# Kernel tuning notes

Measured on AMD Instinct MI355X. Metric: run time of the kernel, lower is better.

## Reference

```python
import jax, jax.numpy as jnp
import numpy as np

B = 4          # per_gpu_batch_size
P = 16         # n_contexts
N = B * P      # fused passage dim = 64
L = 512        # seq_len
H = 768        # hidden_size
S = 16         # sentence spans per passage


def setup_inputs() -> dict:
    key = jax.random.key(0)
    k1, k2, k3 = jax.random.split(key, 3)
    hidden_states = jax.random.normal(k1, (N, L, H), jnp.float32)
    # nn.Linear weight [out, in]; original init std=1.0 saturates tanh, use 0.02 scale for sane numerics
    dense_w = jax.random.normal(k2, (H, H), jnp.float32) * 0.02
    dense_b = jnp.zeros((H,), jnp.float32)
    attention_mask = jnp.ones((N, L), jnp.int32)
    # strictly increasing boundaries -> S non-empty, ragged, contiguous spans per passage
    r = jnp.sort(jax.random.randint(k3, (N, S + 1), 0, L - S), axis=-1) + jnp.arange(S + 1, dtype=jnp.int32)
    spans = jnp.stack([r[:, :-1], r[:, 1:]], axis=-1).astype(jnp.int32)  # [N, S, 2]
    return dict(hidden_states=hidden_states, dense_w=dense_w, dense_b=dense_b,
                attention_mask=attention_mask, spans=spans)


def reference(hidden_states, dense_w, dense_b, attention_mask, spans):
    # sentence_spans branch: token_tensor = hidden_states (all tokens)
    # pooled_output = activation(dense(token_tensor)); cls_norm_type == 'none' -> no norm
    pooled = jnp.tanh(jnp.einsum('nlh,oh->nlo', hidden_states, dense_w) + dense_b)  # [N, L, H]
    pooled_output_passages = pooled[:, 0]  # [N, H]
    # ragged per-span mean pooling, vectorized as a masked segment reduce
    pos = jnp.arange(L, dtype=jnp.int32)                         # [L]
    start = spans[..., 0][..., None]                             # [N, S, 1]
    end = spans[..., 1][..., None]                               # [N, S, 1]
    m = ((pos >= start) & (pos < end)).astype(pooled.dtype)      # [N, S, L]
    sums = jnp.einsum('nsl,nlh->nsh', m, pooled)                 # [N, S, H]
    counts = (spans[..., 1] - spans[..., 0]).astype(pooled.dtype)[..., None]  # [N, S, 1]
    sentence_embeddings = (sums / counts).reshape(N * S, H)      # [N*S, H]
    # all S spans valid per passage -> mask of zeros (0 = valid in original code)
    sentence_mask = jnp.zeros((N, S), jnp.float32)
    return pooled_output_passages, sentence_embeddings, sentence_mask
```

## Files before the change

### kernel.cpp

```cpp
#include <hip/hip_runtime.h>
#include <hip/hip_bf16.h>

#define NPASS 64
#define LSEQ  512
#define HDIM  768
#define NSPAN 16
#define MTOT  (NPASS*LSEQ)
#define OFF_SENT (NPASS*HDIM)
#define OFF_MASK (OFF_SENT + NPASS*NSPAN*HDIM)
#define A_ELEMS (MTOT*HDIM)

#define BN   96
#define NTN  6
#define BK   32
#define NK   (HDIM/BK)
#define NTILES (HDIM/BN)
#define NBLK (NPASS*NTILES)
#define THREADS 512
#define NMT  4

typedef __bf16 bf16x8 __attribute__((ext_vector_type(8)));
typedef __bf16 bf16x4 __attribute__((ext_vector_type(4)));
typedef float  f32x4  __attribute__((ext_vector_type(4)));

__device__ inline unsigned short f2bf(float f) {
  __hip_bfloat16 h = __float2bfloat16(f);
  unsigned short u; __builtin_memcpy(&u, &h, 2); return u;
}

__device__ inline float fast_tanh(float x) {
  const float ax = fabsf(x);
  const float t  = __expf(-2.0f * ax);
  const float r  = (1.0f - t) * __builtin_amdgcn_rcpf(1.0f + t);
  return copysignf(r, x);
}

__device__ inline bf16x8 cvt8(f32x4 lo, f32x4 hi) {
  union { bf16x4 h[2]; bf16x8 v; } u;
  u.h[0] = __builtin_convertvector(lo, bf16x4);
  u.h[1] = __builtin_convertvector(hi, bf16x4);
  return u.v;
}

__global__ __launch_bounds__(256) void convert_a_kernel(
    const float* __restrict__ A, unsigned short* __restrict__ Ab)
{
  const long long i = ((long long)blockIdx.x * 256 + threadIdx.x) * 8;
  const float4 a = *(const float4*)(A + i);
  const float4 b = *(const float4*)(A + i + 4);
  union { unsigned short us[8]; uint4 v; } o;
  o.us[0]=f2bf(a.x); o.us[1]=f2bf(a.y); o.us[2]=f2bf(a.z); o.us[3]=f2bf(a.w);
  o.us[4]=f2bf(b.x); o.us[5]=f2bf(b.y); o.us[6]=f2bf(b.z); o.us[7]=f2bf(b.w);
  *(uint4*)(Ab + i) = o.v;
}

__global__ __launch_bounds__(THREADS, 2) void fused_kernel(
    const unsigned short* __restrict__ Ab,
    const float* __restrict__ W,
    const float* __restrict__ bias,
    const int*   __restrict__ spans,
    float* __restrict__ out)
{
  __shared__ __align__(16) unsigned short Wl[BN * HDIM];
  __shared__ float sent_lds[NSPAN][BN];
  __shared__ float inv_s[NSPAN];
  __shared__ float bias_s[BN];
  __shared__ short sid_l[LSEQ];

  const int tid = threadIdx.x;
  const int b   = blockIdx.x;
  const int xcd = b & 7;
  const int t   = b >> 3;
  const int p   = ((t >> 3) << 3) | xcd;
  const int ntb = t & 7;
  const int tile_n = ntb * BN;


  {
    const float* Wp = W + (size_t)tile_n * HDIM;
    #pragma unroll
    for (int j = 0; j < (BN * (HDIM / 8)) / THREADS; ++j) {
      const int g  = j * THREADS + tid;
      const int wr = g / (HDIM / 8);
      const int kg = g % (HDIM / 8);
      const float* src = Wp + (size_t)wr * HDIM + kg * 8;
      const f32x4 lo = *(const f32x4*)src;
      const f32x4 hi = *(const f32x4*)(src + 4);
      const int kgs = kg ^ (wr & 7);
      *(bf16x8*)(Wl + (size_t)wr * HDIM + kgs * 8) = cvt8(lo, hi);
    }
  }

  {
    int st[NSPAN], en[NSPAN];
    #pragma unroll
    for (int i = 0; i < NSPAN; ++i) {
      st[i] = spans[(p * NSPAN + i) * 2 + 0];
      en[i] = spans[(p * NSPAN + i) * 2 + 1];
    }
    short s = -1;
    #pragma unroll
    for (int i = 0; i < NSPAN; ++i)
      if (tid >= st[i] && tid < en[i]) s = (short)i;
    sid_l[tid] = s;
  }
  if (tid < NSPAN)
    inv_s[tid] = 1.0f / (float)(spans[(p * NSPAN + tid) * 2 + 1] -
                                spans[(p * NSPAN + tid) * 2 + 0]);
  if (tid < BN) bias_s[tid] = bias[tile_n + tid];
  for (int i = tid; i < NSPAN * BN; i += THREADS) (&sent_lds[0][0])[i] = 0.f;

  __syncthreads();

  const int wave = tid >> 6;
  const int lane = tid & 63;
  const int quad = lane >> 4;
  const int lr   = lane & 15;

  const unsigned short* Abp =
      Ab + ((size_t)p * LSEQ + wave * 64 + lr) * HDIM + quad * 8;

  f32x4 acc[NMT][NTN];
  #pragma unroll
  for (int mt = 0; mt < NMT; ++mt)
    #pragma unroll
    for (int nt = 0; nt < NTN; ++nt)
      acc[mt][nt] = (f32x4){0.f, 0.f, 0.f, 0.f};

  bf16x8 a_cur[NMT], a_nxt[NMT];
  #pragma unroll
  for (int mt = 0; mt < NMT; ++mt)
    a_cur[mt] = *(const bf16x8*)(Abp + (size_t)mt * 16 * HDIM);

  #pragma unroll
  for (int k = 0; k < NK; ++k) {
    bf16x8 wf[NTN];
    #pragma unroll
    for (int nt = 0; nt < NTN; ++nt) {
      const int wr = nt * 16 + lr;
      const int kg = (4 * k + quad) ^ (lr & 7);
      wf[nt] = *(const bf16x8*)(Wl + (size_t)wr * HDIM + kg * 8);
    }
    if (k + 1 < NK) {
      #pragma unroll
      for (int mt = 0; mt < NMT; ++mt)
        a_nxt[mt] = *(const bf16x8*)(Abp + (size_t)mt * 16 * HDIM + (k + 1) * BK);
    }
    __builtin_amdgcn_s_setprio(1);
    #pragma unroll
    for (int mt = 0; mt < NMT; ++mt)
      #pragma unroll
      for (int nt = 0; nt < NTN; ++nt)
        acc[mt][nt] = __builtin_amdgcn_mfma_f32_16x16x32_bf16(
            a_cur[mt], wf[nt], acc[mt][nt], 0, 0, 0);
    __builtin_amdgcn_s_setprio(0);
    #pragma unroll
    for (int mt = 0; mt < NMT; ++mt) a_cur[mt] = a_nxt[mt];
  }

  #pragma unroll
  for (int nt = 0; nt < NTN; ++nt) {
    const int col = nt * 16 + lr;
    const float bv = bias_s[col];
    #pragma unroll
    for (int mt = 0; mt < NMT; ++mt) {
      const int rowbase = wave * 64 + mt * 16 + quad * 4;
      int prev = -1; float run = 0.f;
      #pragma unroll
      for (int r = 0; r < 4; ++r) {
        const int row = rowbase + r;
        const float v = fast_tanh(acc[mt][nt][r] + bv);
        if (row == 0) out[(size_t)p * HDIM + tile_n + col] = v;
        const int s = sid_l[row];
        if (s != prev) {
          if (prev >= 0) atomicAdd(&sent_lds[prev][col], run);
          prev = s; run = 0.f;
        }
        run += v;
      }
      if (prev >= 0) atomicAdd(&sent_lds[prev][col], run);
    }
  }
  __syncthreads();

  for (int i = tid; i < NSPAN * BN; i += THREADS) {
    const int s = i / BN, c = i % BN;
    out[OFF_SENT + ((size_t)p * NSPAN + s) * HDIM + tile_n + c] =
        sent_lds[s][c] * inv_s[s];
  }
  if (ntb == 0 && tid < NSPAN) out[OFF_MASK + p * NSPAN + tid] = 0.f;
}

extern "C" void kernel_launch(void* const* d_in, const int* in_sizes, int n_in,
                              void* d_out, int out_size, void* d_ws, size_t ws_size,
                              hipStream_t stream) {
  const float* hs  = (const float*)d_in[0];
  const float* w   = (const float*)d_in[1];
  const float* bsc = (const float*)d_in[2];
  const int* spans = (const int*)d_in[4];

  unsigned short* Ab = (unsigned short*)d_ws;

  convert_a_kernel<<<dim3(A_ELEMS / 8 / 256), dim3(256), 0, stream>>>(hs, Ab);

  fused_kernel<<<dim3(NBLK), dim3(THREADS), 0, stream>>>(
      Ab, w, bsc, spans, (float*)d_out);
}
```

Measured before the change: 237.3 us.

## Pre-convert W to bf16, load via global_load_lds, process two passages per block

W is now converted to bf16 in the same pre-pass as the activations. Each block loads its 96-column W slice into LDS with direct global-to-LDS loads and keeps it resident across two passages. The grid is halved to 256 blocks, which halves the redundant W loads and conversions. The cost is less parallelism: 256 blocks on 256 CUs, each doing serial work with no overlap between passages. There is also an implicit wait on the async LDS loads that relies on the first __syncthreads.

```diff
diff --git a/kernel.cpp b/kernel.cpp
--- a/kernel.cpp
+++ b/kernel.cpp
@@ -9,13 +9,14 @@
 #define OFF_SENT (NPASS*HDIM)
 #define OFF_MASK (OFF_SENT + NPASS*NSPAN*HDIM)
 #define A_ELEMS (MTOT*HDIM)
+#define W_ELEMS (HDIM*HDIM)
 
 #define BN   96
 #define NTN  6
 #define BK   32
 #define NK   (HDIM/BK)
 #define NTILES (HDIM/BN)
-#define NBLK (NPASS*NTILES)
+#define NBLK 256
 #define THREADS 512
 #define NMT  4
 
@@ -35,28 +36,25 @@
   return copysignf(r, x);
 }
 
-__device__ inline bf16x8 cvt8(f32x4 lo, f32x4 hi) {
-  union { bf16x4 h[2]; bf16x8 v; } u;
-  u.h[0] = __builtin_convertvector(lo, bf16x4);
-  u.h[1] = __builtin_convertvector(hi, bf16x4);
-  return u.v;
-}
-
-__global__ __launch_bounds__(256) void convert_a_kernel(
-    const float* __restrict__ A, unsigned short* __restrict__ Ab)
+__global__ __launch_bounds__(256) void convert_kernel(
+    const float* __restrict__ A, const float* __restrict__ W,
+    unsigned short* __restrict__ Ab, unsigned short* __restrict__ Wb)
 {
   const long long i = ((long long)blockIdx.x * 256 + threadIdx.x) * 8;
-  const float4 a = *(const float4*)(A + i);
-  const float4 b = *(const float4*)(A + i + 4);
+  const float* src; unsigned short* dst; long long off;
+  if (i < A_ELEMS) { src = A; dst = Ab; off = i; }
+  else             { src = W; dst = Wb; off = i - A_ELEMS; }
+  const float4 a = *(const float4*)(src + off);
+  const float4 b = *(const float4*)(src + off + 4);
   union { unsigned short us[8]; uint4 v; } o;
   o.us[0]=f2bf(a.x); o.us[1]=f2bf(a.y); o.us[2]=f2bf(a.z); o.us[3]=f2bf(a.w);
   o.us[4]=f2bf(b.x); o.us[5]=f2bf(b.y); o.us[6]=f2bf(b.z); o.us[7]=f2bf(b.w);
-  *(uint4*)(Ab + i) = o.v;
+  *(uint4*)(dst + off) = o.v;
 }
 
 __global__ __launch_bounds__(THREADS, 2) void fused_kernel(
     const unsigned short* __restrict__ Ab,
-    const float* __restrict__ W,
+    const unsigned short* __restrict__ Wb,
     const float* __restrict__ bias,
     const int*   __restrict__ spans,
     float* __restrict__ out)
@@ -71,124 +69,129 @@
   const int b   = blockIdx.x;
   const int xcd = b & 7;
   const int t   = b >> 3;
-  const int p   = ((t >> 3) << 3) | xcd;
+  const int p0  = ((t >> 3) << 3) | xcd;
   const int ntb = t & 7;
   const int tile_n = ntb * BN;
-
-
-  {
-    const float* Wp = W + (size_t)tile_n * HDIM;
-    #pragma unroll
-    for (int j = 0; j < (BN * (HDIM / 8)) / THREADS; ++j) {
-      const int g  = j * THREADS + tid;
-      const int wr = g / (HDIM / 8);
-      const int kg = g % (HDIM / 8);
-      const float* src = Wp + (size_t)wr * HDIM + kg * 8;
-      const f32x4 lo = *(const f32x4*)src;
-      const f32x4 hi = *(const f32x4*)(src + 4);
-      const int kgs = kg ^ (wr & 7);
-      *(bf16x8*)(Wl + (size_t)wr * HDIM + kgs * 8) = cvt8(lo, hi);
-    }
-  }
-
-  {
-    int st[NSPAN], en[NSPAN];
-    #pragma unroll
-    for (int i = 0; i < NSPAN; ++i) {
-      st[i] = spans[(p * NSPAN + i) * 2 + 0];
-      en[i] = spans[(p * NSPAN + i) * 2 + 1];
-    }
-    short s = -1;
-    #pragma unroll
-    for (int i = 0; i < NSPAN; ++i)
-      if (tid >= st[i] && tid < en[i]) s = (short)i;
-    sid_l[tid] = s;
-  }
-  if (tid < NSPAN)
-    inv_s[tid] = 1.0f / (float)(spans[(p * NSPAN + tid) * 2 + 1] -
-                                spans[(p * NSPAN + tid) * 2 + 0]);
-  if (tid < BN) bias_s[tid] = bias[tile_n + tid];
-  for (int i = tid; i < NSPAN * BN; i += THREADS) (&sent_lds[0][0])[i] = 0.f;
-
-  __syncthreads();
 
   const int wave = tid >> 6;
   const int lane = tid & 63;
   const int quad = lane >> 4;
   const int lr   = lane & 15;
 
-  const unsigned short* Abp =
-      Ab + ((size_t)p * LSEQ + wave * 64 + lr) * HDIM + quad * 8;
-
-  f32x4 acc[NMT][NTN];
-  #pragma unroll
-  for (int mt = 0; mt < NMT; ++mt)
-    #pragma unroll
-    for (int nt = 0; nt < NTN; ++nt)
-      acc[mt][nt] = (f32x4){0.f, 0.f, 0.f, 0.f};
-
-  bf16x8 a_cur[NMT], a_nxt[NMT];
-  #pragma unroll
-  for (int mt = 0; mt < NMT; ++mt)
-    a_cur[mt] = *(const bf16x8*)(Abp + (size_t)mt * 16 * HDIM);
-
-  #pragma unroll
-  for (int k = 0; k < NK; ++k) {
-    bf16x8 wf[NTN];
+  {
+    #pragma unroll
+    for (int j = 0; j < (BN * (HDIM / 8)) / THREADS; ++j) {
+      const int gi = j * THREADS + tid;
+      const int wr = gi / (HDIM / 8);
+      const int kg = gi % (HDIM / 8);
+      const unsigned short* src =
+          Wb + (size_t)(tile_n + wr) * HDIM + ((kg ^ (wr & 7)) * 8);
+      __builtin_amdgcn_global_load_lds(
+          (const __attribute__((address_space(1))) void*)src,
+          (__attribute__((address_space(3))) void*)(Wl + (size_t)gi * 8),
+          16, 0, 0);
+    }
+  }
+  if (tid < BN) bias_s[tid] = bias[tile_n + tid];
+
+  for (int pi = 0; pi < 2; ++pi) {
+    const int p = p0 + pi * 32;
+
+    {
+      int st[NSPAN], en[NSPAN];
+      #pragma unroll
+      for (int i = 0; i < NSPAN; ++i) {
+        st[i] = spans[(p * NSPAN + i) * 2 + 0];
+        en[i] = spans[(p * NSPAN + i) * 2 + 1];
+      }
+      short s = -1;
+      #pragma unroll
+      for (int i = 0; i < NSPAN; ++i)
+        if (tid >= st[i] && tid < en[i]) s = (short)i;
+      sid_l[tid] = s;
+    }
+    if (tid < NSPAN)
+      inv_s[tid] = 1.0f / (float)(spans[(p * NSPAN + tid) * 2 + 1] -
+                                  spans[(p * NSPAN + tid) * 2 + 0]);
+    for (int i = tid; i < NSPAN * BN; i += THREADS) (&sent_lds[0][0])[i] = 0.f;
+
+    __syncthreads();
+
+    const unsigned short* Abp =
+        Ab + ((size_t)p * LSEQ + wave * 64 + lr) * HDIM + quad * 8;
+
+    f32x4 acc[NMT][NTN];
+    #pragma unroll
+    for (int mt = 0; mt < NMT; ++mt)
+      #pragma unroll
+      for (int nt = 0; nt < NTN; ++nt)
+        acc[mt][nt] = (f32x4){0.f, 0.f, 0.f, 0.f};
+
+    bf16x8 a_cur[NMT], a_nxt[NMT];
+    #pragma unroll
+    for (int mt = 0; mt < NMT; ++mt)
+      a_cur[mt] = *(const bf16x8*)(Abp + (size_t)mt * 16 * HDIM);
+
+    #pragma unroll
+    for (int k = 0; k < NK; ++k) {
+      bf16x8 wf[NTN];
+      #pragma unroll
+      for (int nt = 0; nt < NTN; ++nt) {
+        const int wr = nt * 16 + lr;
+        const int kg = (4 * k + quad) ^ (lr & 7);
+        wf[nt] = *(const bf16x8*)(Wl + (size_t)wr * HDIM + kg * 8);
+      }
+      if (k + 1 < NK) {
+        #pragma unroll
+        for (int mt = 0; mt < NMT; ++mt)
+          a_nxt[mt] = *(const bf16x8*)(Abp + (size_t)mt * 16 * HDIM + (k + 1) * BK);
+      }
+      __builtin_amdgcn_s_setprio(1);
+      #pragma unroll
+      for (int mt = 0; mt < NMT; ++mt)
+        #pragma unroll
+        for (int nt = 0; nt < NTN; ++nt)
+          acc[mt][nt] = __builtin_amdgcn_mfma_f32_16x16x32_bf16(
+              a_cur[mt], wf[nt], acc[mt][nt], 0, 0, 0);
+      __builtin_amdgcn_s_setprio(0);
+      #pragma unroll
+      for (int mt = 0; mt < NMT; ++mt) a_cur[mt] = a_nxt[mt];
+    }
+
     #pragma unroll
     for (int nt = 0; nt < NTN; ++nt) {
-      const int wr = nt * 16 + lr;
-      const int kg = (4 * k + quad) ^ (lr & 7);
-      wf[nt] = *(const bf16x8*)(Wl + (size_t)wr * HDIM + kg * 8);
-    }
-    if (k + 1 < NK) {
-      #pragma unroll
-      for (int mt = 0; mt < NMT; ++mt)
-        a_nxt[mt] = *(const bf16x8*)(Abp + (size_t)mt * 16 * HDIM + (k + 1) * BK);
-    }
-    __builtin_amdgcn_s_setprio(1);
-    #pragma unroll
-    for (int mt = 0; mt < NMT; ++mt)
-      #pragma unroll
-      for (int nt = 0; nt < NTN; ++nt)
-        acc[mt][nt] = __builtin_amdgcn_mfma_f32_16x16x32_bf16(
-            a_cur[mt], wf[nt], acc[mt][nt], 0, 0, 0);
-    __builtin_amdgcn_s_setprio(0);
-    #pragma unroll
-    for (int mt = 0; mt < NMT; ++mt) a_cur[mt] = a_nxt[mt];
+      const int col = nt * 16 + lr;
+      const float bv = bias_s[col];
+      #pragma unroll
+      for (int mt = 0; mt < NMT; ++mt) {
+        const int rowbase = wave * 64 + mt * 16 + quad * 4;
+        int prev = -1; float run = 0.f;
+        #pragma unroll
+        for (int r = 0; r < 4; ++r) {
+          const int row = rowbase + r;
+          const float v = fast_tanh(acc[mt][nt][r] + bv);
+          if (row == 0) out[(size_t)p * HDIM + tile_n + col] = v;
+          const int s = sid_l[row];
+          if (s != prev) {
+            if (prev >= 0) atomicAdd(&sent_lds[prev][col], run);
+            prev = s; run = 0.f;
+          }
+          run += v;
+        }
+        if (prev >= 0) atomicAdd(&sent_lds[prev][col], run);
+      }
+    }
+    __syncthreads();
+
+    for (int i = tid; i < NSPAN * BN; i += THREADS) {
+      const int s = i / BN, c = i % BN;
+      out[OFF_SENT + ((size_t)p * NSPAN + s) * HDIM + tile_n + c] =
+          sent_lds[s][c] * inv_s[s];
+    }
+    if (ntb == 0 && tid < NSPAN) out[OFF_MASK + p * NSPAN + tid] = 0.f;
+
+    __syncthreads();
   }
-
-  #pragma unroll
-  for (int nt = 0; nt < NTN; ++nt) {
-    const int col = nt * 16 + lr;
-    const float bv = bias_s[col];
-    #pragma unroll
-    for (int mt = 0; mt < NMT; ++mt) {
-      const int rowbase = wave * 64 + mt * 16 + quad * 4;
-      int prev = -1; float run = 0.f;
-      #pragma unroll
-      for (int r = 0; r < 4; ++r) {
-        const int row = rowbase + r;
-        const float v = fast_tanh(acc[mt][nt][r] + bv);
-        if (row == 0) out[(size_t)p * HDIM + tile_n + col] = v;
-        const int s = sid_l[row];
-        if (s != prev) {
-          if (prev >= 0) atomicAdd(&sent_lds[prev][col], run);
-          prev = s; run = 0.f;
-        }
-        run += v;
-      }
-      if (prev >= 0) atomicAdd(&sent_lds[prev][col], run);
-    }
-  }
-  __syncthreads();
-
-  for (int i = tid; i < NSPAN * BN; i += THREADS) {
-    const int s = i / BN, c = i % BN;
-    out[OFF_SENT + ((size_t)p * NSPAN + s) * HDIM + tile_n + c] =
-        sent_lds[s][c] * inv_s[s];
-  }
-  if (ntb == 0 && tid < NSPAN) out[OFF_MASK + p * NSPAN + tid] = 0.f;
 }
 
 extern "C" void kernel_launch(void* const* d_in, const int* in_sizes, int n_in,
@@ -200,9 +203,11 @@
   const int* spans = (const int*)d_in[4];
 
   unsigned short* Ab = (unsigned short*)d_ws;
-
-  convert_a_kernel<<<dim3(A_ELEMS / 8 / 256), dim3(256), 0, stream>>>(hs, Ab);
+  unsigned short* Wb = Ab + A_ELEMS;
+
+  convert_kernel<<<dim3((A_ELEMS + W_ELEMS) / 8 / 256), dim3(256), 0, stream>>>(
+      hs, w, Ab, Wb);
 
   fused_kernel<<<dim3(NBLK), dim3(THREADS), 0, stream>>>(
-      Ab, w, bsc, spans, (float*)d_out);
-}
+      Ab, Wb, bsc, spans, (float*)d_out);
+}
```

Measured after the change: 231.0 us. 2.7% less time.
